# Kernel optimization log

Hardware: AMD Instinct MI355X
Metric: run time of the kernel (lower is better)

Reference implementation:

```python
import jax, jax.numpy as jnp
import numpy as np

SIZE = 11
SIGMA = 1.5
PAD = 5

def _window2d():
    # cv2.getGaussianKernel(11, 1.5): normalized 1D Gaussian, outer product -> 2D window
    x = np.arange(SIZE) - (SIZE - 1) / 2.0
    g = np.exp(-(x * x) / (2.0 * SIGMA * SIGMA))
    g = g / g.sum()
    return jnp.asarray(np.outer(g, g), dtype=jnp.float32)

def _gconv(x, w):
    # x: [H, W]; replicate ('edge') pad by 5 then valid 11x11 correlation (matches torch
    # Conv2d with padding_mode='replicate'); output [H, W]
    xp = jnp.pad(x, PAD, mode='edge')[None, None]  # [1,1,H+10,W+10]
    y = jax.lax.conv_general_dilated(
        xp, w[None, None], window_strides=(1, 1), padding='VALID',
        dimension_numbers=('NCHW', 'OIHW', 'NCHW'))
    return y[0, 0]

def setup_inputs() -> dict:
    key = jax.random.key(0)
    k1, k2 = jax.random.split(key)
    H = W = 4096
    img1 = jax.random.uniform(k1, (H, W), dtype=jnp.float32) * 255.0
    img2 = jax.random.uniform(k2, (H, W), dtype=jnp.float32) * 255.0
    return {"img1": img1, "img2": img2}

def reference(img1, img2):
    w = _window2d()
    C1 = (0.01 * 255) ** 2
    C2 = (0.03 * 255) ** 2
    mu1 = _gconv(img1, w)
    mu2 = _gconv(img2, w)
    mu1_sq = mu1 * mu1
    mu2_sq = mu2 * mu2
    mu1_mu2 = mu1 * mu2
    sigma1_sq = _gconv(img1 * img1, w) - mu1_sq
    sigma2_sq = _gconv(img2 * img2, w) - mu2_sq
    sigma12 = _gconv(img1 * img2, w) - mu1_mu2
    ssim_map = (2 * mu1_mu2 + C1) * (2 * sigma12 + C2) / (
        (mu1_sq + mu2_sq + C1) * (sigma1_sq + sigma2_sq + C2))
    return jnp.mean(ssim_map)
```

## Files before the change

kernel.cpp:

```cpp
#include <hip/hip_runtime.h>
#include <cmath>

#define IMG_H 4096
#define IMG_W 4096
#define GX 8
#define GY 64
#define TCOLS 512
#define R 64
#define NITER (R + 10)
#define SWORDS 528
#define NF4 132
#define NSLOT (2*NF4)

struct GW { float w[11]; };

__device__ __forceinline__ int clampi(int v, int lo, int hi) {
  return v < lo ? lo : (v > hi ? hi : v);
}

__global__ __launch_bounds__(256, 2) void ssim_sweep_kernel(
    const float* __restrict__ img1, const float* __restrict__ img2,
    float* __restrict__ partial, GW gw) {
  __shared__ __align__(16) float sbuf[2][2][SWORDS];

  const int tid  = threadIdx.x;
  const int bx = blockIdx.x, by = blockIdx.y;
  const int c0   = bx * TCOLS;
  const int row0 = by * R;
  const bool edge = (bx == 0) || (bx == GX - 1);

  const int  j0   = tid;
  const bool has2 = (tid < NSLOT - 256);
  const int  j1   = tid + 256;

  auto load_slot = [&](int j, int gr) -> float4 {
    const float* img = (j < NF4) ? img1 : img2;
    int wo = ((j < NF4) ? j : j - NF4) * 4;
    long rowbase = (long)gr * IMG_W;
    int gc = c0 - 8 + wo;
    if (!edge) {
      return *reinterpret_cast<const float4*>(img + rowbase + gc);
    } else {
      float4 v;
      v.x = img[rowbase + clampi(gc + 0, 0, IMG_W - 1)];
      v.y = img[rowbase + clampi(gc + 1, 0, IMG_W - 1)];
      v.z = img[rowbase + clampi(gc + 2, 0, IMG_W - 1)];
      v.w = img[rowbase + clampi(gc + 3, 0, IMG_W - 1)];
      return v;
    }
  };
  auto store_slot = [&](int buf, int j, float4 v) {
    int im = (j < NF4) ? 0 : 1;
    int wo = ((j < NF4) ? j : j - NF4) * 4;
    *reinterpret_cast<float4*>(&sbuf[buf][im][wo]) = v;
  };

  {
    int gr = clampi(row0 - 5, 0, IMG_H - 1);
    float4 v0 = load_slot(j0, gr);
    store_slot(0, j0, v0);
    if (has2) { float4 v1 = load_slot(j1, gr); store_slot(0, j1, v1); }
  }

  float acc[5][11][2];
  #pragma unroll
  for (int ch = 0; ch < 5; ++ch)
    #pragma unroll
    for (int s = 0; s < 11; ++s) { acc[ch][s][0] = 0.f; acc[ch][s][1] = 0.f; }

  float sum = 0.f;
  const int base = 2 * tid + 2;

  for (int g = 0; g < 7; ++g) {
    #pragma unroll
    for (int p = 0; p < 11; ++p) {
      const int i = g * 11 + p;
      if (i < NITER) {
        __syncthreads();

        float4 pre0, pre1;
        const bool pf = (i + 1 < NITER);
        if (pf) {
          int gr = clampi(row0 - 5 + i + 1, 0, IMG_H - 1);
          pre0 = load_slot(j0, gr);
          if (has2) pre1 = load_slot(j1, gr);
        }

        const int cur = i & 1;
        float wa[14], wb[14];
        #pragma unroll
        for (int m = 0; m < 7; ++m) {
          float2 fa = *reinterpret_cast<const float2*>(&sbuf[cur][0][base + 2 * m]);
          float2 fb = *reinterpret_cast<const float2*>(&sbuf[cur][1][base + 2 * m]);
          wa[2 * m] = fa.x; wa[2 * m + 1] = fa.y;
          wb[2 * m] = fb.x; wb[2 * m + 1] = fb.y;
        }

        {
          const int rs = (p + 5) % 11;
          #pragma unroll
          for (int ch = 0; ch < 5; ++ch) { acc[ch][rs][0] = 0.f; acc[ch][rs][1] = 0.f; }
        }

        float h[5][2];
        #pragma unroll
        for (int ch = 0; ch < 5; ++ch) { h[ch][0] = 0.f; h[ch][1] = 0.f; }
        #pragma unroll
        for (int j = 0; j < 11; ++j) {
          const float wj = gw.w[j];
          float a1 = wa[j + 1], a2 = wa[j + 2];
          float b1 = wb[j + 1], b2 = wb[j + 2];
          h[0][0] = fmaf(wj, a1, h[0][0]);      h[0][1] = fmaf(wj, a2, h[0][1]);
          h[1][0] = fmaf(wj, b1, h[1][0]);      h[1][1] = fmaf(wj, b2, h[1][1]);
          h[2][0] = fmaf(wj, a1 * a1, h[2][0]); h[2][1] = fmaf(wj, a2 * a2, h[2][1]);
          h[3][0] = fmaf(wj, b1 * b1, h[3][0]); h[3][1] = fmaf(wj, b2 * b2, h[3][1]);
          h[4][0] = fmaf(wj, a1 * b1, h[4][0]); h[4][1] = fmaf(wj, a2 * b2, h[4][1]);
        }

        #pragma unroll
        for (int d = -5; d <= 5; ++d) {
          const int s = (p + d + 11) % 11;
          const float wd = gw.w[5 - d];
          #pragma unroll
          for (int ch = 0; ch < 5; ++ch) {
            acc[ch][s][0] = fmaf(wd, h[ch][0], acc[ch][s][0]);
            acc[ch][s][1] = fmaf(wd, h[ch][1], acc[ch][s][1]);
          }
        }

        if (i >= 10) {
          const int cs = (p + 6) % 11;
          const float C1 = 6.5025f, C2 = 58.5225f;
          #pragma unroll
          for (int x = 0; x < 2; ++x) {
            float mu1 = acc[0][cs][x], mu2 = acc[1][cs][x];
            float x2 = acc[2][cs][x], y2 = acc[3][cs][x], xy = acc[4][cs][x];
            float mu1s = mu1 * mu1, mu2s = mu2 * mu2, m12 = mu1 * mu2;
            float num = (2.f * m12 + C1) * (2.f * (xy - m12) + C2);
            float den = (mu1s + mu2s + C1) * ((x2 - mu1s) + (y2 - mu2s) + C2);
            sum += num * __builtin_amdgcn_rcpf(den);
          }
        }

        if (pf) {
          store_slot((i + 1) & 1, j0, pre0);
          if (has2) store_slot((i + 1) & 1, j1, pre1);
        }
      }
    }
  }

  #pragma unroll
  for (int off = 32; off > 0; off >>= 1) sum += __shfl_down(sum, off);
  __shared__ float wsum[4];
  if ((tid & 63) == 0) wsum[tid >> 6] = sum;
  __syncthreads();
  if (tid == 0)
    partial[by * GX + bx] = wsum[0] + wsum[1] + wsum[2] + wsum[3];
}

__global__ __launch_bounds__(256) void ssim_reduce_kernel(
    const float* __restrict__ partial, float* __restrict__ out) {
  const int NPART = GX * GY;
  int tid = threadIdx.x;
  double s = (double)partial[tid] + (double)partial[tid + 256];
  #pragma unroll
  for (int off = 32; off > 0; off >>= 1) s += __shfl_down(s, off);
  __shared__ double ws[4];
  if ((tid & 63) == 0) ws[tid >> 6] = s;
  __syncthreads();
  if (tid == 0)
    out[0] = (float)((ws[0] + ws[1] + ws[2] + ws[3]) /
                     ((double)IMG_H * (double)IMG_W));
  (void)NPART;
}

extern "C" void kernel_launch(void* const* d_in, const int* in_sizes, int n_in,
                              void* d_out, int out_size, void* d_ws, size_t ws_size,
                              hipStream_t stream) {
  const float* img1 = (const float*)d_in[0];
  const float* img2 = (const float*)d_in[1];
  float* partial = (float*)d_ws;
  float* out = (float*)d_out;

  GW gw;
  double g[11], s = 0.0;
  for (int i = 0; i < 11; ++i) {
    double x = i - 5.0;
    g[i] = exp(-(x * x) / (2.0 * 1.5 * 1.5));
    s += g[i];
  }
  for (int i = 0; i < 11; ++i) gw.w[i] = (float)(g[i] / s);

  dim3 grid(GX, GY);
  ssim_sweep_kernel<<<grid, 256, 0, stream>>>(img1, img2, partial, gw);
  ssim_reduce_kernel<<<1, 256, 0, stream>>>(partial, out);
}
```

Before: 201.5 us.

## Halve rows per block, raise occupancy, and share squared products across taps

Each block now sweeps 32 output rows instead of 64, doubling the grid to 128 block rows, and the launch bound asks for 4 blocks per SIMD-group instead of 2. The horizontal pass now computes a*a, b*b and a*b once per input element and reuses them for both output columns, cutting redundant multiplies. The reduce kernel loops over the larger partial count. Shorter sweeps add relatively more halo work (10 extra rows per 32 instead of per 64), and the tighter register limit may force spilling of the large accumulator array.

```diff
diff --git a/kernel.cpp b/kernel.cpp
--- a/kernel.cpp
+++ b/kernel.cpp
@@ -4,9 +4,9 @@
 #define IMG_H 4096
 #define IMG_W 4096
 #define GX 8
-#define GY 64
+#define GY 128
 #define TCOLS 512
-#define R 64
+#define R 32
 #define NITER (R + 10)
 #define SWORDS 528
 #define NF4 132
@@ -18,7 +18,7 @@
   return v < lo ? lo : (v > hi ? hi : v);
 }
 
-__global__ __launch_bounds__(256, 2) void ssim_sweep_kernel(
+__global__ __launch_bounds__(256, 4) void ssim_sweep_kernel(
     const float* __restrict__ img1, const float* __restrict__ img2,
     float* __restrict__ partial, GW gw) {
   __shared__ __align__(16) float sbuf[2][2][SWORDS];
@@ -71,7 +71,7 @@
   float sum = 0.f;
   const int base = 2 * tid + 2;
 
-  for (int g = 0; g < 7; ++g) {
+  for (int g = 0; g < 4; ++g) {
     #pragma unroll
     for (int p = 0; p < 11; ++p) {
       const int i = g * 11 + p;
@@ -106,15 +106,25 @@
         #pragma unroll
         for (int ch = 0; ch < 5; ++ch) { h[ch][0] = 0.f; h[ch][1] = 0.f; }
         #pragma unroll
-        for (int j = 0; j < 11; ++j) {
-          const float wj = gw.w[j];
-          float a1 = wa[j + 1], a2 = wa[j + 2];
-          float b1 = wb[j + 1], b2 = wb[j + 2];
-          h[0][0] = fmaf(wj, a1, h[0][0]);      h[0][1] = fmaf(wj, a2, h[0][1]);
-          h[1][0] = fmaf(wj, b1, h[1][0]);      h[1][1] = fmaf(wj, b2, h[1][1]);
-          h[2][0] = fmaf(wj, a1 * a1, h[2][0]); h[2][1] = fmaf(wj, a2 * a2, h[2][1]);
-          h[3][0] = fmaf(wj, b1 * b1, h[3][0]); h[3][1] = fmaf(wj, b2 * b2, h[3][1]);
-          h[4][0] = fmaf(wj, a1 * b1, h[4][0]); h[4][1] = fmaf(wj, a2 * b2, h[4][1]);
+        for (int e = 1; e <= 12; ++e) {
+          const float a = wa[e], b = wb[e];
+          const float aa = a * a, bb = b * b, ab = a * b;
+          if (e <= 11) {
+            const float w0 = gw.w[e - 1];
+            h[0][0] = fmaf(w0, a,  h[0][0]);
+            h[1][0] = fmaf(w0, b,  h[1][0]);
+            h[2][0] = fmaf(w0, aa, h[2][0]);
+            h[3][0] = fmaf(w0, bb, h[3][0]);
+            h[4][0] = fmaf(w0, ab, h[4][0]);
+          }
+          if (e >= 2) {
+            const float w1 = gw.w[e - 2];
+            h[0][1] = fmaf(w1, a,  h[0][1]);
+            h[1][1] = fmaf(w1, b,  h[1][1]);
+            h[2][1] = fmaf(w1, aa, h[2][1]);
+            h[3][1] = fmaf(w1, bb, h[3][1]);
+            h[4][1] = fmaf(w1, ab, h[4][1]);
+          }
         }
 
         #pragma unroll
@@ -163,7 +173,9 @@
     const float* __restrict__ partial, float* __restrict__ out) {
   const int NPART = GX * GY;
   int tid = threadIdx.x;
-  double s = (double)partial[tid] + (double)partial[tid + 256];
+  double s = 0.0;
+  #pragma unroll
+  for (int q = 0; q < NPART / 256; ++q) s += (double)partial[tid + q * 256];
   #pragma unroll
   for (int off = 32; off > 0; off >>= 1) s += __shfl_down(s, off);
   __shared__ double ws[4];
@@ -172,7 +184,6 @@
   if (tid == 0)
     out[0] = (float)((ws[0] + ws[1] + ws[2] + ws[3]) /
                      ((double)IMG_H * (double)IMG_W));
-  (void)NPART;
 }
 
 extern "C" void kernel_launch(void* const* d_in, const int* in_sizes, int n_in,
```

Measured after the change: 614.4 us. 3.05x slower.
